# Optimization experiments

Measured on AMD Instinct MI355X. Metric: run time of the kernel, lower is better.

Reference implementation:

```python
import jax, jax.numpy as jnp
import numpy as np

N_NODES = 100000
N_HYPEREDGES = 20000
NNZ = 600000
D = 128


def setup_inputs() -> dict:
    key = jax.random.key(0)
    k = jax.random.split(key, 6)
    s = 1.0 / np.sqrt(D)
    x = jax.random.normal(k[0], (N_NODES, D), jnp.float32)
    node_idx = jax.random.randint(k[1], (NNZ,), 0, N_NODES, dtype=jnp.int64 if jax.config.jax_enable_x64 else jnp.int32)
    edge_idx = jax.random.randint(k[2], (NNZ,), 0, N_HYPEREDGES, dtype=jnp.int64 if jax.config.jax_enable_x64 else jnp.int32)
    conv_W = jax.random.uniform(k[3], (D, D), jnp.float32, -s, s)
    conv_b = jnp.zeros((D,), jnp.float32)
    res_W = jax.random.uniform(k[4], (D, D), jnp.float32, -s, s)
    res_b = jax.random.uniform(k[5], (D,), jnp.float32, -s, s)
    return {"x": x, "node_idx": node_idx, "edge_idx": edge_idx,
            "conv_W": conv_W, "conv_b": conv_b, "res_W": res_W, "res_b": res_b}


def hypergraph_conv(x, node_idx, edge_idx, W, b):
    # PyG HypergraphConv (no attention, unit hyperedge weights):
    #   out = D^{-1} H B^{-1} H^T (x W) + b
    y = x @ W                                                      # [N, D]
    ones = jnp.ones(node_idx.shape, dtype=y.dtype)
    deg_n = jax.ops.segment_sum(ones, node_idx, num_segments=N_NODES)        # node degree
    deg_e = jax.ops.segment_sum(ones, edge_idx, num_segments=N_HYPEREDGES)   # hyperedge size
    inv_n = jnp.where(deg_n > 0, 1.0 / deg_n, 0.0)
    inv_e = jnp.where(deg_e > 0, 1.0 / deg_e, 0.0)
    # node -> hyperedge aggregation, normalized by B^{-1}
    e_feat = jax.ops.segment_sum(y[node_idx], edge_idx, num_segments=N_HYPEREDGES)
    e_feat = e_feat * inv_e[:, None]                               # [E, D]
    # hyperedge -> node aggregation, normalized by D^{-1}
    out = jax.ops.segment_sum(e_feat[edge_idx], node_idx, num_segments=N_NODES)
    out = out * inv_n[:, None]                                     # [N, D]
    return out + b


def reference(x, node_idx, edge_idx, conv_W, conv_b, res_W, res_b):
    h = hypergraph_conv(x, node_idx, edge_idx, conv_W, conv_b)     # layer_num = 1
    return (x @ res_W + res_b) + h                                 # residual Linear + conv out
```

## Files before the change

### kernel.cpp

```cpp
#include <hip/hip_runtime.h>

#define N_NODES 100000
#define N_EDGES 20000
#define NNZ_C   600000
#define D 128

typedef short bf16x8 __attribute__((ext_vector_type(8)));
typedef float f32x4  __attribute__((ext_vector_type(4)));

__device__ __forceinline__ unsigned short f2bf(float f) {
    unsigned int u = __float_as_uint(f);
    u = (u + 0x7fffu + ((u >> 16) & 1u)) >> 16;
    return (unsigned short)u;
}
__device__ __forceinline__ float bf2f(unsigned short h) {
    return __uint_as_float((unsigned int)h << 16);
}
__device__ __forceinline__ unsigned int pk_trunc(float lo, float hi) {
    return __builtin_amdgcn_perm(__float_as_uint(hi), __float_as_uint(lo),
                                 0x07060302);
}

#define CH 4096
#define NCHUNK 147
#define CONVB 256
#define EBW 32
#define NBE 625
#define ECAP 1280
#define NBW 128
#define NBN 782
#define NCAP 1024
#define PADI 32
#define GCUR_INTS ((NBE + NBN) * PADI)

#define GT 64
#define XPAD 136
#define NTILES ((N_NODES + GT - 1) / GT)
#define TPB 3
#define GEMM_BLKS ((NTILES + TPB - 1) / TPB)

__global__ __launch_bounds__(512) void fused_bin_conv(
    const float* __restrict__ x,
    const int* __restrict__ nidx, const int* __restrict__ eidx,
    unsigned short* __restrict__ xb,
    int* __restrict__ bucket_e, int* __restrict__ bucket_n,
    int* __restrict__ gcur_e, int* __restrict__ gcur_n) {
    __shared__ int srt[CH];
    __shared__ int cnt[NBN], lbase[NBN], gbase[NBN], cur[NBN];
    const int bid = blockIdx.x;
    const int tid = threadIdx.x;

    if (bid >= NCHUNK) {
        const int total8 = N_NODES * D / 8;
        for (int g = (bid - NCHUNK) * 512 + tid; g < total8;
             g += CONVB * 512) {
            const float4 a = *(const float4*)(x + (size_t)g * 8);
            const float4 c = *(const float4*)(x + (size_t)g * 8 + 4);
            uint4 v;
            v.x = pk_trunc(a.x, a.y);
            v.y = pk_trunc(a.z, a.w);
            v.z = pk_trunc(c.x, c.y);
            v.w = pk_trunc(c.z, c.w);
            *(uint4*)(xb + (size_t)g * 8) = v;
        }
        return;
    }

    const int j0 = bid * CH;
    const int jn = (j0 + CH < NNZ_C) ? CH : NNZ_C - j0;
#pragma unroll
    for (int s = 0; s < 2; ++s) {
        const int nb = s ? NBN : NBE;
        int* gc = s ? gcur_n : gcur_e;
        int* dst = s ? bucket_n : bucket_e;
        const int cap = s ? NCAP : ECAP;
        for (int i = tid; i < nb; i += 512) cnt[i] = 0;
        __syncthreads();
        for (int i = tid; i < jn; i += 512) {
            const int id = s ? nidx[j0 + i] : eidx[j0 + i];
            atomicAdd(&cnt[s ? (id >> 7) : (id >> 5)], 1);
        }
        __syncthreads();
        if (tid < 64) {
            int loc[13];
            int ssum = 0;
            const int k0 = tid * 13;
#pragma unroll
            for (int k = 0; k < 13; ++k) {
                const int idx = k0 + k;
                loc[k] = ssum;
                if (idx < nb) ssum += cnt[idx];
            }
            int v = ssum;
#pragma unroll
            for (int off = 1; off < 64; off <<= 1) {
                const int t = __shfl_up(v, off);
                if (tid >= off) v += t;
            }
            const int base = v - ssum;
#pragma unroll
            for (int k = 0; k < 13; ++k) {
                const int idx = k0 + k;
                if (idx < nb) {
                    lbase[idx] = base + loc[k];
                    cur[idx] = base + loc[k];
                }
            }
        }
        __syncthreads();
        for (int i = tid; i < nb; i += 512)
            gbase[i] = cnt[i] ? atomicAdd(&gc[i * PADI], cnt[i]) : 0;
        __syncthreads();
        for (int i = tid; i < jn; i += 512) {
            const int e = eidx[j0 + i], n = nidx[j0 + i];
            const int b = s ? (n >> 7) : (e >> 5);
            const unsigned pk = s ? (unsigned)(((n & 127) << 15) | e)
                                  : (unsigned)(((e & 31) << 17) | n);
            const int pos = atomicAdd(&cur[b], 1);
            srt[pos] = (int)(pk | ((unsigned)b << 22));
        }
        __syncthreads();
        for (int i = tid; i < jn; i += 512) {
            const unsigned v = (unsigned)srt[i];
            const int b = v >> 22;
            const int o2 = gbase[b] + (i - lbase[b]);
            if (o2 < cap) dst[b * cap + o2] = (int)(v & 0x3FFFFFu);
        }
        __syncthreads();
    }
}

__global__ __launch_bounds__(512) void edge_mean(
    const int* __restrict__ bucket_e, const int* __restrict__ gcur_e,
    const unsigned short* __restrict__ xb, unsigned short* __restrict__ sb) {
    __shared__ int raw[ECAP];
    __shared__ int srt[ECAP];
    __shared__ int cnt[EBW + 1];
    __shared__ int cur[EBW];
    const int tid = threadIdx.x;
    const int b = blockIdx.x;
    int W = gcur_e[b * PADI];
    if (W > ECAP) W = ECAP;
    if (tid <= EBW) cnt[tid] = 0;
    __syncthreads();
    const int* src = bucket_e + b * ECAP;
    for (int i = tid; i < W; i += 512) {
        const int p = src[i];
        raw[i] = p;
        atomicAdd(&cnt[p >> 17], 1);
    }
    __syncthreads();
    if (tid < EBW) {
        const int c = cnt[tid];
        int v = c;
#pragma unroll
        for (int off = 1; off < EBW; off <<= 1) {
            const int t = __shfl_up(v, off);
            if (tid >= off) v += t;
        }
        cnt[tid] = v - c;
        cur[tid] = v - c;
        if (tid == EBW - 1) cnt[EBW] = v;
    }
    __syncthreads();
    for (int i = tid; i < W; i += 512) {
        const int p = raw[i];
        const int pos = atomicAdd(&cur[p >> 17], 1);
        srt[pos] = p & 0x1FFFF;
    }
    __syncthreads();

    const int g = tid >> 4;
    const int l = tid & 15;
    const int beg = cnt[g], end = cnt[g + 1];
    float acc[8] = {};
    int j = beg;
    for (; j + 4 <= end; j += 4) {
        const int n0 = srt[j], n1 = srt[j + 1];
        const int n2 = srt[j + 2], n3 = srt[j + 3];
        const bf16x8 p0 = *(const bf16x8*)(xb + (size_t)n0 * D + l * 8);
        const bf16x8 p1 = *(const bf16x8*)(xb + (size_t)n1 * D + l * 8);
        const bf16x8 p2 = *(const bf16x8*)(xb + (size_t)n2 * D + l * 8);
        const bf16x8 p3 = *(const bf16x8*)(xb + (size_t)n3 * D + l * 8);
#pragma unroll
        for (int i = 0; i < 8; ++i)
            acc[i] += (bf2f((unsigned short)p0[i]) + bf2f((unsigned short)p1[i]))
                    + (bf2f((unsigned short)p2[i]) + bf2f((unsigned short)p3[i]));
    }
    for (; j < end; ++j) {
        const bf16x8 p = *(const bf16x8*)(xb + (size_t)srt[j] * D + l * 8);
#pragma unroll
        for (int i = 0; i < 8; ++i) acc[i] += bf2f((unsigned short)p[i]);
    }
    const int deg = end - beg;
    const float inv = deg ? 1.f / (float)deg : 0.f;
    bf16x8 o;
#pragma unroll
    for (int i = 0; i < 8; ++i) o[i] = (short)f2bf(acc[i] * inv);
    *(bf16x8*)(sb + (size_t)(b * EBW + g) * D + l * 8) = o;
}

__global__ __launch_bounds__(512) void node_mean(
    const int* __restrict__ bucket_n, const int* __restrict__ gcur_n,
    const unsigned short* __restrict__ sb, unsigned short* __restrict__ zb) {
    __shared__ int raw[NCAP];
    __shared__ int srt[NCAP];
    __shared__ int cnt[NBW + 1];
    __shared__ int cur[NBW];
    const int tid = threadIdx.x;
    const int b = blockIdx.x;
    int W = gcur_n[b * PADI];
    if (W > NCAP) W = NCAP;
    if (tid <= NBW) cnt[tid] = 0;
    __syncthreads();
    const int* src = bucket_n + b * NCAP;
    for (int i = tid; i < W; i += 512) {
        const int p = src[i];
        raw[i] = p;
        atomicAdd(&cnt[p >> 15], 1);
    }
    __syncthreads();
    if (tid < 64) {
        const int a0 = cnt[tid * 2], a1 = cnt[tid * 2 + 1];
        const int ssum = a0 + a1;
        int v = ssum;
#pragma unroll
        for (int off = 1; off < 64; off <<= 1) {
            const int t = __shfl_up(v, off);
            if (tid >= off) v += t;
        }
        const int base = v - ssum;
        cnt[tid * 2] = base;     cur[tid * 2] = base;
        cnt[tid * 2 + 1] = base + a0; cur[tid * 2 + 1] = base + a0;
        if (tid == 63) cnt[NBW] = v;
    }
    __syncthreads();
    for (int i = tid; i < W; i += 512) {
        const int p = raw[i];
        const int pos = atomicAdd(&cur[p >> 15], 1);
        srt[pos] = p & 0x7FFF;
    }
    __syncthreads();

    const int g = tid >> 4;
    const int l = tid & 15;
#pragma unroll
    for (int u = 0; u < 4; ++u) {
        const int nl = g * 4 + u;
        const int n = b * NBW + nl;
        if (n >= N_NODES) continue;
        const int beg = cnt[nl], end = cnt[nl + 1];
        float acc[8] = {};
        int j = beg;
        for (; j + 2 <= end; j += 2) {
            const int e0 = srt[j], e1 = srt[j + 1];
            const bf16x8 p0 = *(const bf16x8*)(sb + (size_t)e0 * D + l * 8);
            const bf16x8 p1 = *(const bf16x8*)(sb + (size_t)e1 * D + l * 8);
#pragma unroll
            for (int i = 0; i < 8; ++i)
                acc[i] += bf2f((unsigned short)p0[i]) + bf2f((unsigned short)p1[i]);
        }
        if (j < end) {
            const bf16x8 p = *(const bf16x8*)(sb + (size_t)srt[j] * D + l * 8);
#pragma unroll
            for (int i = 0; i < 8; ++i) acc[i] += bf2f((unsigned short)p[i]);
        }
        const int deg = end - beg;
        const float inv = deg ? 1.f / (float)deg : 0.f;
        bf16x8 o;
#pragma unroll
        for (int i = 0; i < 8; ++i) o[i] = (short)f2bf(acc[i] * inv);
        *(bf16x8*)(zb + (size_t)n * D + l * 8) = o;
    }
}

__global__ __launch_bounds__(512) void final_gemm(
    const unsigned short* __restrict__ zb, const unsigned short* __restrict__ xb,
    const float* __restrict__ cW, const float* __restrict__ rW,
    const float* __restrict__ cbias, const float* __restrict__ rbias,
    float* __restrict__ out) {
    __shared__ unsigned short zs[GT * XPAD];
    __shared__ unsigned short xs[GT * XPAD];

    const int tid  = threadIdx.x;
    const int w    = tid >> 6;
    const int lane = tid & 63;
    const int quad = lane >> 4;
    const int l16  = lane & 15;
    const int f0   = w * 16;

    const int f = f0 + l16;
    bf16x8 Ac[4], Ar[4];
#pragma unroll
    for (int kc = 0; kc < 4; ++kc)
#pragma unroll
        for (int u = 0; u < 8; ++u) {
            const int k = kc * 32 + quad * 8 + u;
            Ac[kc][u] = (short)f2bf(cW[(size_t)k * D + f]);
            Ar[kc][u] = (short)f2bf(rW[(size_t)k * D + f]);
        }
    const float4 cb4 = *(const float4*)(cbias + f0 + quad * 4);
    const float4 rb4 = *(const float4*)(rbias + f0 + quad * 4);
    const float4 bias = {cb4.x + rb4.x, cb4.y + rb4.y,
                         cb4.z + rb4.z, cb4.w + rb4.w};

    const int r0 = tid >> 3;
    const int qp = tid & 7;

    for (int tt = 0; tt < TPB; ++tt) {
        const int t = blockIdx.x * TPB + tt;
        if (t >= NTILES) break;
        __syncthreads();
        {
            int n = t * GT + r0;
            if (n >= N_NODES) n = N_NODES - 1;
            const uint4* sz = (const uint4*)(zb + (size_t)n * D + qp * 16);
            const uint4* sx = (const uint4*)(xb + (size_t)n * D + qp * 16);
            uint4* dz = (uint4*)(zs + r0 * XPAD + qp * 16);
            uint4* dx = (uint4*)(xs + r0 * XPAD + qp * 16);
            dz[0] = sz[0]; dz[1] = sz[1];
            dx[0] = sx[0]; dx[1] = sx[1];
        }
        __syncthreads();
        f32x4 acc[4] = {};
#pragma unroll
        for (int g = 0; g < 4; ++g)
#pragma unroll
            for (int kc = 0; kc < 4; ++kc) {
                const int ro = (g * 16 + l16) * XPAD + kc * 32 + quad * 8;
                const bf16x8 Bz = *(const bf16x8*)(zs + ro);
                const bf16x8 Bx = *(const bf16x8*)(xs + ro);
                acc[g] = __builtin_amdgcn_mfma_f32_16x16x32_bf16(Ac[kc], Bz, acc[g], 0, 0, 0);
                acc[g] = __builtin_amdgcn_mfma_f32_16x16x32_bf16(Ar[kc], Bx, acc[g], 0, 0, 0);
            }
        const int nbase = t * GT;
#pragma unroll
        for (int g = 0; g < 4; ++g) {
            const int n = nbase + g * 16 + l16;
            if (n >= N_NODES) continue;
            float4 o;
            o.x = acc[g][0] + bias.x;
            o.y = acc[g][1] + bias.y;
            o.z = acc[g][2] + bias.z;
            o.w = acc[g][3] + bias.w;
            *(float4*)(out + (size_t)n * D + f0 + quad * 4) = o;
        }
    }
}

extern "C" void kernel_launch(void* const* d_in, const int* in_sizes, int n_in,
                              void* d_out, int out_size, void* d_ws,
                              size_t ws_size, hipStream_t stream) {
    const float* x  = (const float*)d_in[0];
    const int* nidx = (const int*)d_in[1];
    const int* eidx = (const int*)d_in[2];
    const float* cW = (const float*)d_in[3];
    const float* cb = (const float*)d_in[4];
    const float* rW = (const float*)d_in[5];
    const float* rb = (const float*)d_in[6];
    float* out = (float*)d_out;

    char* ws = (char*)d_ws;
    size_t off = 0;
    auto alloc = [&](size_t bytes) {
        size_t o = off;
        off += (bytes + 255) & ~(size_t)255;
        return o;
    };
    unsigned short* xb = (unsigned short*)(ws + alloc((size_t)N_NODES * D * 2));
    unsigned short* sb = (unsigned short*)(ws + alloc((size_t)N_EDGES * D * 2));
    unsigned short* zb = (unsigned short*)(ws + alloc((size_t)N_NODES * D * 2));
    int* bucket_e = (int*)(ws + alloc((size_t)NBE * ECAP * 4));
    int* bucket_n = (int*)(ws + alloc((size_t)NBN * NCAP * 4));
    int* gcur     = (int*)(ws + alloc((size_t)GCUR_INTS * 4));
    int* gcur_e = gcur;
    int* gcur_n = gcur + NBE * PADI;

    hipMemsetAsync(gcur, 0, (size_t)GCUR_INTS * 4, stream);

    fused_bin_conv<<<NCHUNK + CONVB, 512, 0, stream>>>(
        x, nidx, eidx, xb, bucket_e, bucket_n, gcur_e, gcur_n);

    edge_mean<<<NBE, 512, 0, stream>>>(bucket_e, gcur_e, xb, sb);
    node_mean<<<NBN, 512, 0, stream>>>(bucket_n, gcur_n, sb, zb);
    final_gemm<<<GEMM_BLKS, 512, 0, stream>>>(zb, xb, cW, rW, cb, rb, out);
}
```

Measured before the change: 193.3 us.

## Fuse node-mean aggregation into final GEMM via shared memory tile

Merges the node_mean and final_gemm kernels so each 128-node bucket computes its mean edge features directly into LDS and immediately runs the MFMA GEMM on them. This removes the zb intermediate round trip through global memory and one kernel launch. Edge_mean also gains an 8-way unrolled gather loop and node aggregation goes to 4-way unroll for more memory-level parallelism. In exchange, each block reloads weights into registers (782 blocks versus fewer before), and LDS usage and register pressure rise, which may lower occupancy.

```diff
diff --git a/kernel.cpp b/kernel.cpp
--- a/kernel.cpp
+++ b/kernel.cpp
@@ -36,8 +36,6 @@
 #define GT 64
 #define XPAD 136
 #define NTILES ((N_NODES + GT - 1) / GT)
-#define TPB 3
-#define GEMM_BLKS ((NTILES + TPB - 1) / TPB)
 
 __global__ __launch_bounds__(512) void fused_bin_conv(
     const float* __restrict__ x,
@@ -175,6 +173,20 @@
     const int beg = cnt[g], end = cnt[g + 1];
     float acc[8] = {};
     int j = beg;
+    for (; j + 8 <= end; j += 8) {
+        bf16x8 p[8];
+#pragma unroll
+        for (int q = 0; q < 8; ++q)
+            p[q] = *(const bf16x8*)(xb + (size_t)srt[j + q] * D + l * 8);
+#pragma unroll
+        for (int i = 0; i < 8; ++i) {
+            float t0 = bf2f((unsigned short)p[0][i]) + bf2f((unsigned short)p[1][i]);
+            float t1 = bf2f((unsigned short)p[2][i]) + bf2f((unsigned short)p[3][i]);
+            float t2 = bf2f((unsigned short)p[4][i]) + bf2f((unsigned short)p[5][i]);
+            float t3 = bf2f((unsigned short)p[6][i]) + bf2f((unsigned short)p[7][i]);
+            acc[i] += (t0 + t1) + (t2 + t3);
+        }
+    }
     for (; j + 4 <= end; j += 4) {
         const int n0 = srt[j], n1 = srt[j + 1];
         const int n2 = srt[j + 2], n3 = srt[j + 3];
@@ -200,15 +212,21 @@
     *(bf16x8*)(sb + (size_t)(b * EBW + g) * D + l * 8) = o;
 }
 
-__global__ __launch_bounds__(512) void node_mean(
+__global__ __launch_bounds__(512, 4) void node_gemm(
     const int* __restrict__ bucket_n, const int* __restrict__ gcur_n,
-    const unsigned short* __restrict__ sb, unsigned short* __restrict__ zb) {
+    const unsigned short* __restrict__ sb, const unsigned short* __restrict__ xb,
+    const float* __restrict__ cW, const float* __restrict__ rW,
+    const float* __restrict__ cbias, const float* __restrict__ rbias,
+    float* __restrict__ out) {
     __shared__ int raw[NCAP];
     __shared__ int srt[NCAP];
     __shared__ int cnt[NBW + 1];
     __shared__ int cur[NBW];
+    __shared__ unsigned short zs[NBW * XPAD];
+    __shared__ unsigned short xs[GT * XPAD];
     const int tid = threadIdx.x;
     const int b = blockIdx.x;
+
     int W = gcur_n[b * PADI];
     if (W > NCAP) W = NCAP;
     if (tid <= NBW) cnt[tid] = 0;
@@ -230,7 +248,7 @@
             if (tid >= off) v += t;
         }
         const int base = v - ssum;
-        cnt[tid * 2] = base;     cur[tid * 2] = base;
+        cnt[tid * 2] = base;          cur[tid * 2] = base;
         cnt[tid * 2 + 1] = base + a0; cur[tid * 2 + 1] = base + a0;
         if (tid == 63) cnt[NBW] = v;
     }
@@ -242,54 +260,47 @@
     }
     __syncthreads();
 
-    const int g = tid >> 4;
-    const int l = tid & 15;
-#pragma unroll
-    for (int u = 0; u < 4; ++u) {
-        const int nl = g * 4 + u;
-        const int n = b * NBW + nl;
-        if (n >= N_NODES) continue;
-        const int beg = cnt[nl], end = cnt[nl + 1];
-        float acc[8] = {};
-        int j = beg;
-        for (; j + 2 <= end; j += 2) {
-            const int e0 = srt[j], e1 = srt[j + 1];
-            const bf16x8 p0 = *(const bf16x8*)(sb + (size_t)e0 * D + l * 8);
-            const bf16x8 p1 = *(const bf16x8*)(sb + (size_t)e1 * D + l * 8);
-#pragma unroll
-            for (int i = 0; i < 8; ++i)
-                acc[i] += bf2f((unsigned short)p0[i]) + bf2f((unsigned short)p1[i]);
-        }
-        if (j < end) {
-            const bf16x8 p = *(const bf16x8*)(sb + (size_t)srt[j] * D + l * 8);
-#pragma unroll
-            for (int i = 0; i < 8; ++i) acc[i] += bf2f((unsigned short)p[i]);
-        }
-        const int deg = end - beg;
-        const float inv = deg ? 1.f / (float)deg : 0.f;
-        bf16x8 o;
-#pragma unroll
-        for (int i = 0; i < 8; ++i) o[i] = (short)f2bf(acc[i] * inv);
-        *(bf16x8*)(zb + (size_t)n * D + l * 8) = o;
-    }
-}
-
-__global__ __launch_bounds__(512) void final_gemm(
-    const unsigned short* __restrict__ zb, const unsigned short* __restrict__ xb,
-    const float* __restrict__ cW, const float* __restrict__ rW,
-    const float* __restrict__ cbias, const float* __restrict__ rbias,
-    float* __restrict__ out) {
-    __shared__ unsigned short zs[GT * XPAD];
-    __shared__ unsigned short xs[GT * XPAD];
-
-    const int tid  = threadIdx.x;
+    {
+        const int g = tid >> 4;
+        const int l = tid & 15;
+#pragma unroll
+        for (int u = 0; u < 4; ++u) {
+            const int nl = g * 4 + u;
+            const int beg = cnt[nl], end = cnt[nl + 1];
+            float acc[8] = {};
+            int j = beg;
+            for (; j + 4 <= end; j += 4) {
+                const int e0 = srt[j], e1 = srt[j + 1];
+                const int e2 = srt[j + 2], e3 = srt[j + 3];
+                const bf16x8 p0 = *(const bf16x8*)(sb + (size_t)e0 * D + l * 8);
+                const bf16x8 p1 = *(const bf16x8*)(sb + (size_t)e1 * D + l * 8);
+                const bf16x8 p2 = *(const bf16x8*)(sb + (size_t)e2 * D + l * 8);
+                const bf16x8 p3 = *(const bf16x8*)(sb + (size_t)e3 * D + l * 8);
+#pragma unroll
+                for (int i = 0; i < 8; ++i)
+                    acc[i] += (bf2f((unsigned short)p0[i]) + bf2f((unsigned short)p1[i]))
+                            + (bf2f((unsigned short)p2[i]) + bf2f((unsigned short)p3[i]));
+            }
+            for (; j < end; ++j) {
+                const bf16x8 p = *(const bf16x8*)(sb + (size_t)srt[j] * D + l * 8);
+#pragma unroll
+                for (int i = 0; i < 8; ++i) acc[i] += bf2f((unsigned short)p[i]);
+            }
+            const int deg = end - beg;
+            const float inv = deg ? 1.f / (float)deg : 0.f;
+            bf16x8 o;
+#pragma unroll
+            for (int i = 0; i < 8; ++i) o[i] = (short)f2bf(acc[i] * inv);
+            *(bf16x8*)(zs + nl * XPAD + l * 8) = o;
+        }
+    }
+
     const int w    = tid >> 6;
     const int lane = tid & 63;
     const int quad = lane >> 4;
     const int l16  = lane & 15;
     const int f0   = w * 16;
-
-    const int f = f0 + l16;
+    const int f    = f0 + l16;
     bf16x8 Ac[4], Ar[4];
 #pragma unroll
     for (int kc = 0; kc < 4; ++kc)
@@ -307,18 +318,14 @@
     const int r0 = tid >> 3;
     const int qp = tid & 7;
 
-    for (int tt = 0; tt < TPB; ++tt) {
-        const int t = blockIdx.x * TPB + tt;
-        if (t >= NTILES) break;
+#pragma unroll
+    for (int h = 0; h < 2; ++h) {
         __syncthreads();
         {
-            int n = t * GT + r0;
+            int n = b * NBW + h * GT + r0;
             if (n >= N_NODES) n = N_NODES - 1;
-            const uint4* sz = (const uint4*)(zb + (size_t)n * D + qp * 16);
             const uint4* sx = (const uint4*)(xb + (size_t)n * D + qp * 16);
-            uint4* dz = (uint4*)(zs + r0 * XPAD + qp * 16);
             uint4* dx = (uint4*)(xs + r0 * XPAD + qp * 16);
-            dz[0] = sz[0]; dz[1] = sz[1];
             dx[0] = sx[0]; dx[1] = sx[1];
         }
         __syncthreads();
@@ -327,16 +334,15 @@
         for (int g = 0; g < 4; ++g)
 #pragma unroll
             for (int kc = 0; kc < 4; ++kc) {
-                const int ro = (g * 16 + l16) * XPAD + kc * 32 + quad * 8;
-                const bf16x8 Bz = *(const bf16x8*)(zs + ro);
-                const bf16x8 Bx = *(const bf16x8*)(xs + ro);
+                const int ko = kc * 32 + quad * 8;
+                const bf16x8 Bz = *(const bf16x8*)(zs + (h * GT + g * 16 + l16) * XPAD + ko);
+                const bf16x8 Bx = *(const bf16x8*)(xs + (g * 16 + l16) * XPAD + ko);
                 acc[g] = __builtin_amdgcn_mfma_f32_16x16x32_bf16(Ac[kc], Bz, acc[g], 0, 0, 0);
                 acc[g] = __builtin_amdgcn_mfma_f32_16x16x32_bf16(Ar[kc], Bx, acc[g], 0, 0, 0);
             }
-        const int nbase = t * GT;
 #pragma unroll
         for (int g = 0; g < 4; ++g) {
-            const int n = nbase + g * 16 + l16;
+            const int n = b * NBW + h * GT + g * 16 + l16;
             if (n >= N_NODES) continue;
             float4 o;
             o.x = acc[g][0] + bias.x;
@@ -369,7 +375,6 @@
     };
     unsigned short* xb = (unsigned short*)(ws + alloc((size_t)N_NODES * D * 2));
     unsigned short* sb = (unsigned short*)(ws + alloc((size_t)N_EDGES * D * 2));
-    unsigned short* zb = (unsigned short*)(ws + alloc((size_t)N_NODES * D * 2));
     int* bucket_e = (int*)(ws + alloc((size_t)NBE * ECAP * 4));
     int* bucket_n = (int*)(ws + alloc((size_t)NBN * NCAP * 4));
     int* gcur     = (int*)(ws + alloc((size_t)GCUR_INTS * 4));
@@ -382,6 +387,6 @@
         x, nidx, eidx, xb, bucket_e, bucket_n, gcur_e, gcur_n);
 
     edge_mean<<<NBE, 512, 0, stream>>>(bucket_e, gcur_e, xb, sb);
-    node_mean<<<NBN, 512, 0, stream>>>(bucket_n, gcur_n, sb, zb);
-    final_gemm<<<GEMM_BLKS, 512, 0, stream>>>(zb, xb, cW, rW, cb, rb, out);
-}
+    node_gemm<<<NBN, 512, 0, stream>>>(bucket_n, gcur_n, sb, xb,
+                                       cW, rW, cb, rb, out);
+}
```

New measurement: 190.7 us. No clear change (-1.3%).
